# Optimization experiments

Measured on AMD Instinct MI355X. Metric: run time of the kernel, lower is better.

Reference implementation:

```python
import jax, jax.numpy as jnp
import numpy as np

HEADS = 4
DIM_HEAD = 128


def setup_inputs() -> dict:
    key = jax.random.key(0)
    k1, k2, k3, k4, k5 = jax.random.split(key, 5)
    dim = 256
    f, h, w = 8, 14, 14
    inner = HEADS * DIM_HEAD
    scale = DIM_HEAD ** -0.5
    fmap = jax.random.normal(k1, (8, dim, f, h, w), dtype=jnp.float32)
    # Conv3d 1x1x1, no bias -> plain channel matmul weight [3*inner, dim]
    W_qkv = jax.random.normal(k2, (3 * inner, dim), dtype=jnp.float32) * (dim ** -0.5)
    pos_f = jax.random.normal(k3, (f, DIM_HEAD), dtype=jnp.float32) * scale
    pos_h = jax.random.normal(k4, (h, DIM_HEAD), dtype=jnp.float32) * scale
    pos_w = jax.random.normal(k5, (w, DIM_HEAD), dtype=jnp.float32) * scale
    return {"fmap": fmap, "W_qkv": W_qkv, "pos_f": pos_f, "pos_h": pos_h, "pos_w": pos_w}


def reference(fmap, W_qkv, pos_f, pos_h, pos_w):
    b, c, f, h, w = fmap.shape
    n = f * h * w
    scale = DIM_HEAD ** -0.5
    # 1x1x1 Conv3d == channel matmul
    qkv = jnp.einsum('bcfhw,oc->bofhw', fmap, W_qkv)  # [b, 3*inner, f, h, w]
    q, k, v = jnp.split(qkv, 3, axis=1)
    # 'b (h d) x y z -> b h (x y z) d'
    def to_heads(t):
        return t.reshape(b, HEADS, DIM_HEAD, n).transpose(0, 1, 3, 2)
    q, k, v = to_heads(q), to_heads(k), to_heads(v)
    q = q * scale
    # additive absolute positional embedding [n, d]
    emb = (pos_f[:, None, None, :] + pos_h[None, :, None, :] + pos_w[None, None, :, :]).reshape(n, DIM_HEAD)
    sim = jnp.einsum('bhid,bhjd->bhij', q, k) + jnp.einsum('bhid,jd->bhij', q, emb)
    attn = jax.nn.softmax(sim, axis=-1)
    out = jnp.einsum('bhij,bhjd->bhid', attn, v)  # [b, heads, n, d]
    # 'b h (x y z) d -> b (h d) x y z'
    out = out.transpose(0, 1, 3, 2).reshape(b, HEADS * DIM_HEAD, f, h, w)
    return out
```

## Files before the change

kernel.cpp:

```cpp
#include <hip/hip_runtime.h>
#include <hip/hip_bf16.h>
#include <cstdint>

#define NPOS 1568
#define NQPAD 1664
#define NKVT 25
#define DHEAD 128
#define DIM 256
#define NHEADS 4
#define SCALE_Q (0.08838834764831845f * 1.4426950408889634f)

typedef __bf16 bf16x8 __attribute__((ext_vector_type(8)));
typedef float f32x4 __attribute__((ext_vector_type(4)));
typedef float f32x16 __attribute__((ext_vector_type(16)));
typedef unsigned short u16;
typedef u16 u16x8 __attribute__((ext_vector_type(8)));

__device__ __forceinline__ u16 f2bf(float x) {
  union { float f; unsigned int u; } v; v.f = x;
  return (u16)((v.u + 0x7FFFu + ((v.u >> 16) & 1u)) >> 16);
}

__device__ __forceinline__ unsigned cvtpk(float a, float b) {
  unsigned r;
  asm("v_cvt_pk_bf16_f32 %0, %1, %2" : "=v"(r) : "v"(a), "v"(b));
  return r;
}

__device__ __forceinline__ void gload_lds16(const void* g, void* s) {
  __builtin_amdgcn_global_load_lds(
      (const __attribute__((address_space(1))) unsigned*)g,
      (__attribute__((address_space(3))) unsigned*)s, 16, 0, 0);
}

__device__ __forceinline__ f32x16 zero16() {
  f32x16 v;
#pragma unroll
  for (int i = 0; i < 16; ++i) v[i] = 0.f;
  return v;
}

__global__ __launch_bounds__(256) void emb_kernel(
    const float* __restrict__ pf, const float* __restrict__ ph,
    const float* __restrict__ pw, float* __restrict__ emb) {
  int idx = blockIdx.x * 256 + threadIdx.x;
  int pos = idx >> 7, d = idx & 127;
  int jf = pos / 196; int r = pos - jf * 196; int jh = r / 14; int jw = r - jh * 14;
  emb[idx] = pf[jf * 128 + d] + ph[jh * 128 + d] + pw[jw * 128 + d];
}

__device__ __forceinline__ bf16x8 lds_frag64(const u16* base, int row, int ks, int l15, int g) {
  int r = row + l15;
  int off = r * 128 + ((ks * 64 + g * 16) ^ ((r & 7) << 4));
  return *(const bf16x8*)((const char*)base + off);
}

union PSMem {
  struct { u16 wt[64 * 64]; u16 xt[64 * 64]; } s;
  float o_lds[64 * 68];
};

__global__ __launch_bounds__(256) void proj_kernel(
    const float* __restrict__ fmap, const float* __restrict__ W,
    const float* __restrict__ emb, u16* __restrict__ qws, char* __restrict__ tiles) {
  __shared__ PSMem sm;
  const int tid = threadIdx.x;
  const int lane = tid & 63, w = tid >> 6, l15 = lane & 15, g = lane >> 4;
  const int pos0 = blockIdx.x * 64, o0 = blockIdx.y * 64, b = blockIdx.z;

  f32x4 acc[4];
#pragma unroll
  for (int t = 0; t < 4; ++t) acc[t] = (f32x4){0.f, 0.f, 0.f, 0.f};

  for (int c0 = 0; c0 < DIM; c0 += 64) {
    {
      int r = tid >> 2, c16 = (tid & 3) * 16;
      const float* src = W + (o0 + r) * DIM + c0 + c16;
      float4 f0 = *(const float4*)(src + 0);
      float4 f1 = *(const float4*)(src + 4);
      float4 f2 = *(const float4*)(src + 8);
      float4 f3 = *(const float4*)(src + 12);
      u16x8 a, bvv;
      a[0]=f2bf(f0.x); a[1]=f2bf(f0.y); a[2]=f2bf(f0.z); a[3]=f2bf(f0.w);
      a[4]=f2bf(f1.x); a[5]=f2bf(f1.y); a[6]=f2bf(f1.z); a[7]=f2bf(f1.w);
      bvv[0]=f2bf(f2.x); bvv[1]=f2bf(f2.y); bvv[2]=f2bf(f2.z); bvv[3]=f2bf(f2.w);
      bvv[4]=f2bf(f3.x); bvv[5]=f2bf(f3.y); bvv[6]=f2bf(f3.z); bvv[7]=f2bf(f3.w);
      int byte0 = r * 128 + ((c16 * 2) ^ ((r & 7) << 4));
      int byte1 = r * 128 + ((c16 * 2 + 16) ^ ((r & 7) << 4));
      *(u16x8*)((char*)sm.s.wt + byte0) = a;
      *(u16x8*)((char*)sm.s.wt + byte1) = bvv;
    }
#pragma unroll
    for (int it = 0; it < 2; ++it) {
      int cl = (tid >> 3) + it * 32;
      int p8 = (tid & 7) * 8;
      int gp = pos0 + p8;
      if (gp > NPOS - 8) gp = NPOS - 8;
      const float* src = fmap + ((size_t)(b * DIM + c0 + cl)) * NPOS + gp;
      float4 f0 = *(const float4*)(src + 0);
      float4 f1 = *(const float4*)(src + 4);
      float vals[8] = {f0.x, f0.y, f0.z, f0.w, f1.x, f1.y, f1.z, f1.w};
#pragma unroll
      for (int i = 0; i < 8; ++i) {
        int pl = p8 + i;
        int byte = pl * 128 + ((cl * 2) ^ ((pl & 7) << 4));
        *(u16*)((char*)sm.s.xt + byte) = f2bf(vals[i]);
      }
    }
    __syncthreads();
#pragma unroll
    for (int ks = 0; ks < 2; ++ks) {
      bf16x8 aw = lds_frag64(sm.s.wt, w * 16, ks, l15, g);
#pragma unroll
      for (int t = 0; t < 4; ++t) {
        bf16x8 bx = lds_frag64(sm.s.xt, t * 16, ks, l15, g);
        acc[t] = __builtin_amdgcn_mfma_f32_16x16x32_bf16(aw, bx, acc[t], 0, 0, 0);
      }
    }
    __syncthreads();
  }

  const int sec = o0 >> 9;
  const int head = (o0 >> 7) & 3;
  const int dbase = o0 & 127;
  const int bh = b * NHEADS + head;

  if (sec < 2) {
#pragma unroll
    for (int t = 0; t < 4; ++t)
#pragma unroll
      for (int r = 0; r < 4; ++r)
        sm.o_lds[(t * 16 + l15) * 68 + (w * 16 + 4 * g + r)] = acc[t][r];
  } else {
#pragma unroll
    for (int t = 0; t < 4; ++t)
#pragma unroll
      for (int r = 0; r < 4; ++r)
        sm.o_lds[(w * 16 + 4 * g + r) * 68 + (t * 16 + l15)] = acc[t][r];
  }
  __syncthreads();

  if (sec == 0) {
#pragma unroll
    for (int it = 0; it < 2; ++it) {
      int cid = tid + it * 256;
      int p = cid >> 3, c8 = (cid & 7) * 8;
      int gpos = pos0 + p;
      u16x8 o;
      if (gpos < NPOS) {
#pragma unroll
        for (int i = 0; i < 8; ++i) o[i] = f2bf(sm.o_lds[p * 68 + c8 + i] * SCALE_Q);
      } else {
#pragma unroll
        for (int i = 0; i < 8; ++i) o[i] = 0;
      }
      *(u16x8*)(qws + ((size_t)bh * NQPAD + gpos) * DHEAD + dbase + c8) = o;
    }
  } else if (sec == 1) {
    if (pos0 < NKVT * 64) {
#pragma unroll
      for (int it = 0; it < 2; ++it) {
        int cid = tid + it * 256;
        int p = cid >> 3, c8 = (cid & 7) * 8;
        int gpos = pos0 + p;
        u16x8 o;
        if (gpos < NPOS) {
          const float* eb = emb + (size_t)gpos * DHEAD + dbase + c8;
#pragma unroll
          for (int i = 0; i < 8; ++i) o[i] = f2bf(sm.o_lds[p * 68 + c8 + i] + eb[i]);
        } else {
#pragma unroll
          for (int i = 0; i < 8; ++i) o[i] = 0;
        }
        int jt = gpos >> 6, jl = gpos & 63;
        char* dst = tiles + ((size_t)(bh * NKVT + jt)) * 32768 + jl * 256 +
                    (((dbase + c8) * 2) ^ ((jl & 7) << 4));
        *(u16x8*)dst = o;
      }
    }
  } else {
    if (pos0 < NKVT * 64) {
      int jt = pos0 >> 6;
#pragma unroll
      for (int it = 0; it < 2; ++it) {
        int cid = tid + it * 256;
        int r = cid >> 3, p8 = (cid & 7) * 8;
        int d = dbase + r;
        u16x8 o;
        if (pos0 + p8 < NPOS) {
#pragma unroll
          for (int i = 0; i < 8; ++i) o[i] = f2bf(sm.o_lds[r * 68 + p8 + i]);
        } else {
#pragma unroll
          for (int i = 0; i < 8; ++i) o[i] = 0;
        }
        char* dst = tiles + ((size_t)(bh * NKVT + jt)) * 32768 + 16384 + d * 128 +
                    ((p8 * 2) ^ ((d & 7) << 4));
        *(u16x8*)dst = o;
      }
    }
  }
}

__global__ __launch_bounds__(256) void attn_kernel(
    const u16* __restrict__ qws, const char* __restrict__ tiles,
    float* __restrict__ out) {
  __shared__ char smem[65536];
  const int tid = threadIdx.x;
  const int lane = tid & 63, w = tid >> 6;
  const int l31 = lane & 31, hi = lane >> 5;
  const int bh = blockIdx.y, b = bh >> 2, h = bh & 3;
  const int q0 = blockIdx.x * 128;
  const int rho = (l31 & 0x13) | ((l31 & 4) << 1) | ((l31 & 8) >> 1);

  bf16x8 qf[8];
  {
    const u16* qp = qws + ((size_t)bh * NQPAD + q0 + w * 32 + l31) * DHEAD + 8 * hi;
#pragma unroll
    for (int kk = 0; kk < 8; ++kk) qf[kk] = *(const bf16x8*)(qp + kk * 16);
  }

  f32x16 oacc[4];
#pragma unroll
  for (int dt = 0; dt < 4; ++dt) oacc[dt] = zero16();
  float m = -1e30f, l = 0.f;

  const size_t tbase = (size_t)bh * NKVT * 32768;

  {
    const char* src = tiles + tbase + w * 8192 + lane * 16;
    char* dst = smem + w * 8192;
#pragma unroll
    for (int i = 0; i < 8; ++i) gload_lds16(src + i * 1024, dst + i * 1024);
  }
  __syncthreads();

  int cur = 0;
  for (int jt = 0; jt < NKVT; ++jt) {
    if (jt + 1 < NKVT) {
      const char* src = tiles + tbase + (size_t)(jt + 1) * 32768 + w * 8192 + lane * 16;
      char* dst = smem + (cur ^ 1) * 32768 + w * 8192;
#pragma unroll
      for (int i = 0; i < 8; ++i) gload_lds16(src + i * 1024, dst + i * 1024);
    }
    const char* kt = smem + cur * 32768;
    const char* vt = kt + 16384;
    const bool full = (jt < NKVT - 1);

    f32x16 sc0 = zero16(), sc1 = zero16();
    {
      int row = rho, swz = (row & 7) << 4;
#pragma unroll
      for (int kk = 0; kk < 8; ++kk) {
        bf16x8 ka = *(const bf16x8*)(kt + row * 256 + ((kk * 32 + 16 * hi) ^ swz));
        sc0 = __builtin_amdgcn_mfma_f32_32x32x16_bf16(ka, qf[kk], sc0, 0, 0, 0);
      }
    }
    if (full) {
      int row = 32 + rho, swz = (row & 7) << 4;
#pragma unroll
      for (int kk = 0; kk < 8; ++kk) {
        bf16x8 ka = *(const bf16x8*)(kt + row * 256 + ((kk * 32 + 16 * hi) ^ swz));
        sc1 = __builtin_amdgcn_mfma_f32_32x32x16_bf16(ka, qf[kk], sc1, 0, 0, 0);
      }
    }

    float pm = -1e30f;
#pragma unroll
    for (int i = 0; i < 16; ++i) pm = fmaxf(pm, sc0[i]);
    if (full) {
#pragma unroll
      for (int i = 0; i < 16; ++i) pm = fmaxf(pm, sc1[i]);
    }
    pm = fmaxf(pm, __shfl_xor(pm, 32));
    if (!__all(pm <= m + 8.f)) {
      float mn = fmaxf(m, pm);
      float al = exp2f(m - mn);
      m = mn;
      l *= al;
#pragma unroll
      for (int dt = 0; dt < 4; ++dt)
#pragma unroll
        for (int i = 0; i < 16; ++i) oacc[dt][i] *= al;
    }
    float lac = 0.f;
#pragma unroll
    for (int i = 0; i < 16; ++i) { sc0[i] = exp2f(sc0[i] - m); lac += sc0[i]; }
    if (full) {
#pragma unroll
      for (int i = 0; i < 16; ++i) { sc1[i] = exp2f(sc1[i] - m); lac += sc1[i]; }
    }
    l += lac;

    {
      union { unsigned u[4]; bf16x8 v; } pb0, pb1;
      pb0.u[0] = cvtpk(sc0[0], sc0[1]);  pb0.u[1] = cvtpk(sc0[2], sc0[3]);
      pb0.u[2] = cvtpk(sc0[4], sc0[5]);  pb0.u[3] = cvtpk(sc0[6], sc0[7]);
      pb1.u[0] = cvtpk(sc0[8], sc0[9]);  pb1.u[1] = cvtpk(sc0[10], sc0[11]);
      pb1.u[2] = cvtpk(sc0[12], sc0[13]); pb1.u[3] = cvtpk(sc0[14], sc0[15]);
#pragma unroll
      for (int dt = 0; dt < 4; ++dt) {
        int row = dt * 32 + l31, swz = (row & 7) << 4;
        bf16x8 va0 = *(const bf16x8*)(vt + row * 128 + ((16 * hi) ^ swz));
        oacc[dt] = __builtin_amdgcn_mfma_f32_32x32x16_bf16(va0, pb0.v, oacc[dt], 0, 0, 0);
        bf16x8 va1 = *(const bf16x8*)(vt + row * 128 + ((32 + 16 * hi) ^ swz));
        oacc[dt] = __builtin_amdgcn_mfma_f32_32x32x16_bf16(va1, pb1.v, oacc[dt], 0, 0, 0);
      }
    }
    if (full) {
      union { unsigned u[4]; bf16x8 v; } pb0, pb1;
      pb0.u[0] = cvtpk(sc1[0], sc1[1]);  pb0.u[1] = cvtpk(sc1[2], sc1[3]);
      pb0.u[2] = cvtpk(sc1[4], sc1[5]);  pb0.u[3] = cvtpk(sc1[6], sc1[7]);
      pb1.u[0] = cvtpk(sc1[8], sc1[9]);  pb1.u[1] = cvtpk(sc1[10], sc1[11]);
      pb1.u[2] = cvtpk(sc1[12], sc1[13]); pb1.u[3] = cvtpk(sc1[14], sc1[15]);
#pragma unroll
      for (int dt = 0; dt < 4; ++dt) {
        int row = dt * 32 + l31, swz = (row & 7) << 4;
        bf16x8 va0 = *(const bf16x8*)(vt + row * 128 + ((64 + 16 * hi) ^ swz));
        oacc[dt] = __builtin_amdgcn_mfma_f32_32x32x16_bf16(va0, pb0.v, oacc[dt], 0, 0, 0);
        bf16x8 va1 = *(const bf16x8*)(vt + row * 128 + ((96 + 16 * hi) ^ swz));
        oacc[dt] = __builtin_amdgcn_mfma_f32_32x32x16_bf16(va1, pb1.v, oacc[dt], 0, 0, 0);
      }
    }
    __syncthreads();
    cur ^= 1;
  }

  float lt = l + __shfl_xor(l, 32);
  float linv = 1.f / lt;
  const int q = q0 + w * 32 + l31;
  if (q < NPOS) {
    float* ob = out + (size_t)(b * 512 + h * 128) * NPOS + q;
#pragma unroll
    for (int dt = 0; dt < 4; ++dt)
#pragma unroll
      for (int r = 0; r < 16; ++r) {
        int d = dt * 32 + (r & 3) + 8 * (r >> 2) + 4 * hi;
        ob[(size_t)d * NPOS] = oacc[dt][r] * linv;
      }
  }
}

extern "C" void kernel_launch(void* const* d_in, const int* in_sizes, int n_in,
                              void* d_out, int out_size, void* d_ws, size_t ws_size,
                              hipStream_t stream) {
  const float* fmap = (const float*)d_in[0];
  const float* W    = (const float*)d_in[1];
  const float* pf   = (const float*)d_in[2];
  const float* ph   = (const float*)d_in[3];
  const float* pw   = (const float*)d_in[4];
  float* out = (float*)d_out;

  char* ws = (char*)d_ws;
  const size_t QSZ = (size_t)32 * NQPAD * DHEAD * 2;
  const size_t TSZ = (size_t)32 * NKVT * 32768;
  u16* qws = (u16*)ws;
  char* tiles = ws + QSZ;
  float* emb = (float*)(ws + QSZ + TSZ);

  emb_kernel<<<dim3(784), dim3(256), 0, stream>>>(pf, ph, pw, emb);
  proj_kernel<<<dim3(26, 24, 8), dim3(256), 0, stream>>>(fmap, W, emb, qws, tiles);
  attn_kernel<<<dim3(13, 32), dim3(256), 0, stream>>>(qws, tiles, out);
}
```

Baseline: 137.1 us.

## Pre-convert operands, enlarge projection tiles, split attention KV across warp groups

Adds kernels that convert W to bf16 and transpose fmap into a position-major bf16 layout, staged in the output buffer as scratch. The projection GEMM becomes a 128x128 tile per block that loads MFMA fragments straight from global memory, with no LDS staging or per-chunk barriers. The attention kernel moves to 512 threads, and two warp groups each take half of every KV tile; their softmax states and accumulators are merged through LDS at the end. Block indices are also remapped for batch interleaving. This targets conversion overhead and raises parallelism in attention, at the cost of extra launches, a final merge step, and reliance on output-buffer scratch being overwritten in time.

```diff
diff --git a/kernel.cpp b/kernel.cpp
--- a/kernel.cpp
+++ b/kernel.cpp
@@ -7,7 +7,6 @@
 #define NKVT 25
 #define DHEAD 128
 #define DIM 256
-#define NHEADS 4
 #define SCALE_Q (0.08838834764831845f * 1.4426950408889634f)
 
 typedef __bf16 bf16x8 __attribute__((ext_vector_type(8)));
@@ -15,11 +14,6 @@
 typedef float f32x16 __attribute__((ext_vector_type(16)));
 typedef unsigned short u16;
 typedef u16 u16x8 __attribute__((ext_vector_type(8)));
-
-__device__ __forceinline__ u16 f2bf(float x) {
-  union { float f; unsigned int u; } v; v.f = x;
-  return (u16)((v.u + 0x7FFFu + ((v.u >> 16) & 1u)) >> 16);
-}
 
 __device__ __forceinline__ unsigned cvtpk(float a, float b) {
   unsigned r;
@@ -49,173 +43,200 @@
   emb[idx] = pf[jf * 128 + d] + ph[jh * 128 + d] + pw[jw * 128 + d];
 }
 
-__device__ __forceinline__ bf16x8 lds_frag64(const u16* base, int row, int ks, int l15, int g) {
-  int r = row + l15;
-  int off = r * 128 + ((ks * 64 + g * 16) ^ ((r & 7) << 4));
-  return *(const bf16x8*)((const char*)base + off);
-}
-
-union PSMem {
-  struct { u16 wt[64 * 64]; u16 xt[64 * 64]; } s;
-  float o_lds[64 * 68];
-};
-
-__global__ __launch_bounds__(256) void proj_kernel(
-    const float* __restrict__ fmap, const float* __restrict__ W,
+__global__ __launch_bounds__(256) void wconv_kernel(
+    const float* __restrict__ W, u16* __restrict__ Wbf) {
+  int i8 = (blockIdx.x * 256 + threadIdx.x) * 8;
+  float4 f0 = *(const float4*)(W + i8);
+  float4 f1 = *(const float4*)(W + i8 + 4);
+  union { unsigned u[4]; u16x8 v; } o;
+  o.u[0] = cvtpk(f0.x, f0.y); o.u[1] = cvtpk(f0.z, f0.w);
+  o.u[2] = cvtpk(f1.x, f1.y); o.u[3] = cvtpk(f1.z, f1.w);
+  *(u16x8*)(Wbf + i8) = o.v;
+}
+
+__global__ __launch_bounds__(256) void ftrans_kernel(
+    const float* __restrict__ fmap, u16* __restrict__ fmapT) {
+  __shared__ float t[64][68];
+  const int tid = threadIdx.x;
+  const int pos0 = blockIdx.x * 64, c0 = blockIdx.y * 64, b = blockIdx.z;
+  const int cl = tid >> 3, p8 = (tid & 7) * 8;
+  const bool pv = (pos0 + p8) < NPOS;
+#pragma unroll
+  for (int half = 0; half < 2; ++half) {
+    int c = cl + half * 32;
+    float4 f0 = {0.f, 0.f, 0.f, 0.f}, f1 = {0.f, 0.f, 0.f, 0.f};
+    if (pv) {
+      const float* src = fmap + ((size_t)(b * DIM + c0 + c)) * NPOS + pos0 + p8;
+      f0 = *(const float4*)src;
+      f1 = *(const float4*)(src + 4);
+    }
+    *(float4*)&t[c][p8] = f0;
+    *(float4*)&t[c][p8 + 4] = f1;
+  }
+  __syncthreads();
+  const int pl = tid >> 2, c16 = (tid & 3) * 16;
+  const int gpos = pos0 + pl;
+  union { unsigned u[8]; } o;
+  if (gpos < NPOS) {
+#pragma unroll
+    for (int i = 0; i < 8; ++i) o.u[i] = cvtpk(t[c16 + 2 * i][pl], t[c16 + 2 * i + 1][pl]);
+  } else {
+#pragma unroll
+    for (int i = 0; i < 8; ++i) o.u[i] = 0;
+  }
+  u16* dst = fmapT + ((size_t)b * NQPAD + gpos) * DIM + c0 + c16;
+  *(uint4*)(dst) = *(uint4*)&o.u[0];
+  *(uint4*)(dst + 8) = *(uint4*)&o.u[4];
+}
+
+__global__ __launch_bounds__(256, 4) void proj_kernel(
+    const u16* __restrict__ Wbf, const u16* __restrict__ fmapT,
     const float* __restrict__ emb, u16* __restrict__ qws, char* __restrict__ tiles) {
-  __shared__ PSMem sm;
+  __shared__ float ot[64][132];
   const int tid = threadIdx.x;
-  const int lane = tid & 63, w = tid >> 6, l15 = lane & 15, g = lane >> 4;
-  const int pos0 = blockIdx.x * 64, o0 = blockIdx.y * 64, b = blockIdx.z;
-
-  f32x4 acc[4];
-#pragma unroll
-  for (int t = 0; t < 4; ++t) acc[t] = (f32x4){0.f, 0.f, 0.f, 0.f};
-
-  for (int c0 = 0; c0 < DIM; c0 += 64) {
-    {
-      int r = tid >> 2, c16 = (tid & 3) * 16;
-      const float* src = W + (o0 + r) * DIM + c0 + c16;
-      float4 f0 = *(const float4*)(src + 0);
-      float4 f1 = *(const float4*)(src + 4);
-      float4 f2 = *(const float4*)(src + 8);
-      float4 f3 = *(const float4*)(src + 12);
-      u16x8 a, bvv;
-      a[0]=f2bf(f0.x); a[1]=f2bf(f0.y); a[2]=f2bf(f0.z); a[3]=f2bf(f0.w);
-      a[4]=f2bf(f1.x); a[5]=f2bf(f1.y); a[6]=f2bf(f1.z); a[7]=f2bf(f1.w);
-      bvv[0]=f2bf(f2.x); bvv[1]=f2bf(f2.y); bvv[2]=f2bf(f2.z); bvv[3]=f2bf(f2.w);
-      bvv[4]=f2bf(f3.x); bvv[5]=f2bf(f3.y); bvv[6]=f2bf(f3.z); bvv[7]=f2bf(f3.w);
-      int byte0 = r * 128 + ((c16 * 2) ^ ((r & 7) << 4));
-      int byte1 = r * 128 + ((c16 * 2 + 16) ^ ((r & 7) << 4));
-      *(u16x8*)((char*)sm.s.wt + byte0) = a;
-      *(u16x8*)((char*)sm.s.wt + byte1) = bvv;
-    }
-#pragma unroll
-    for (int it = 0; it < 2; ++it) {
-      int cl = (tid >> 3) + it * 32;
-      int p8 = (tid & 7) * 8;
-      int gp = pos0 + p8;
-      if (gp > NPOS - 8) gp = NPOS - 8;
-      const float* src = fmap + ((size_t)(b * DIM + c0 + cl)) * NPOS + gp;
-      float4 f0 = *(const float4*)(src + 0);
-      float4 f1 = *(const float4*)(src + 4);
-      float vals[8] = {f0.x, f0.y, f0.z, f0.w, f1.x, f1.y, f1.z, f1.w};
-#pragma unroll
-      for (int i = 0; i < 8; ++i) {
-        int pl = p8 + i;
-        int byte = pl * 128 + ((cl * 2) ^ ((pl & 7) << 4));
-        *(u16*)((char*)sm.s.xt + byte) = f2bf(vals[i]);
-      }
-    }
-    __syncthreads();
-#pragma unroll
-    for (int ks = 0; ks < 2; ++ks) {
-      bf16x8 aw = lds_frag64(sm.s.wt, w * 16, ks, l15, g);
-#pragma unroll
-      for (int t = 0; t < 4; ++t) {
-        bf16x8 bx = lds_frag64(sm.s.xt, t * 16, ks, l15, g);
-        acc[t] = __builtin_amdgcn_mfma_f32_16x16x32_bf16(aw, bx, acc[t], 0, 0, 0);
-      }
-    }
-    __syncthreads();
-  }
-
-  const int sec = o0 >> 9;
-  const int head = (o0 >> 7) & 3;
-  const int dbase = o0 & 127;
-  const int bh = b * NHEADS + head;
+  const int lane = tid & 63, w = tid >> 6;
+  const int l15 = lane & 15, g = lane >> 4;
+  const int wid = blockIdx.x;
+  const int b = wid & 7;
+  const int gq = wid >> 3;
+  const int o0 = (gq / 13) * 128;
+  const int pos0 = (gq % 13) * 128;
+  const int wo = (w & 1) * 64, wp = (w >> 1) * 64;
+
+  f32x4 acc[4][4];
+#pragma unroll
+  for (int i = 0; i < 4; ++i)
+#pragma unroll
+    for (int j = 0; j < 4; ++j) acc[i][j] = (f32x4){0.f, 0.f, 0.f, 0.f};
+
+  const u16* Ab = Wbf + (size_t)(o0 + wo + l15) * DIM + g * 8;
+  const u16* Bb = fmapT + ((size_t)b * NQPAD + pos0 + wp + l15) * DIM + g * 8;
+#pragma unroll 2
+  for (int c0 = 0; c0 < DIM; c0 += 32) {
+    bf16x8 a[4], bb[4];
+#pragma unroll
+    for (int t = 0; t < 4; ++t) a[t] = *(const bf16x8*)(Ab + (size_t)t * 16 * DIM + c0);
+#pragma unroll
+    for (int t = 0; t < 4; ++t) bb[t] = *(const bf16x8*)(Bb + (size_t)t * 16 * DIM + c0);
+#pragma unroll
+    for (int i = 0; i < 4; ++i)
+#pragma unroll
+      for (int j = 0; j < 4; ++j)
+        acc[i][j] = __builtin_amdgcn_mfma_f32_16x16x32_bf16(a[i], bb[j], acc[i][j], 0, 0, 0);
+  }
+
+  const int sec = o0 >> 9, head = (o0 >> 7) & 3, bh = b * 4 + head;
 
   if (sec < 2) {
 #pragma unroll
-    for (int t = 0; t < 4; ++t)
-#pragma unroll
-      for (int r = 0; r < 4; ++r)
-        sm.o_lds[(t * 16 + l15) * 68 + (w * 16 + 4 * g + r)] = acc[t][r];
+    for (int ph = 0; ph < 2; ++ph) {
+      __syncthreads();
+      if (wp == ph * 64) {
+#pragma unroll
+        for (int i = 0; i < 4; ++i)
+#pragma unroll
+          for (int j = 0; j < 4; ++j)
+#pragma unroll
+            for (int r = 0; r < 4; ++r)
+              ot[j * 16 + l15][wo + i * 16 + 4 * g + r] = acc[i][j][r];
+      }
+      __syncthreads();
+      const int pl = tid >> 2, c32 = (tid & 3) * 32;
+      const int gpos = pos0 + ph * 64 + pl;
+      float v[32];
+#pragma unroll
+      for (int i = 0; i < 32; ++i) v[i] = ot[pl][c32 + i];
+      if (sec == 0) {
+#pragma unroll
+        for (int q = 0; q < 4; ++q) {
+          union { unsigned u[4]; u16x8 h; } o8;
+#pragma unroll
+          for (int i = 0; i < 4; ++i)
+            o8.u[i] = cvtpk(v[q * 8 + 2 * i] * SCALE_Q, v[q * 8 + 2 * i + 1] * SCALE_Q);
+          *(u16x8*)(qws + ((size_t)bh * NQPAD + gpos) * DHEAD + c32 + q * 8) = o8.h;
+        }
+      } else {
+        if (gpos < NKVT * 64) {
+          if (gpos < NPOS) {
+            const float* eb = emb + (size_t)gpos * DHEAD + c32;
+#pragma unroll
+            for (int i = 0; i < 8; ++i) {
+              float4 e = *(const float4*)(eb + i * 4);
+              v[i * 4 + 0] += e.x; v[i * 4 + 1] += e.y;
+              v[i * 4 + 2] += e.z; v[i * 4 + 3] += e.w;
+            }
+          }
+          const int jt = gpos >> 6, jl = gpos & 63;
+          char* base = tiles + ((size_t)(bh * NKVT + jt)) * 32768 + jl * 256;
+          const int swz = (jl & 7) << 4;
+#pragma unroll
+          for (int q = 0; q < 4; ++q) {
+            union { unsigned u[4]; u16x8 h; } o8;
+#pragma unroll
+            for (int i = 0; i < 4; ++i)
+              o8.u[i] = cvtpk(v[q * 8 + 2 * i], v[q * 8 + 2 * i + 1]);
+            *(u16x8*)(base + (((c32 + q * 8) * 2) ^ swz)) = o8.h;
+          }
+        }
+      }
+    }
   } else {
 #pragma unroll
-    for (int t = 0; t < 4; ++t)
-#pragma unroll
-      for (int r = 0; r < 4; ++r)
-        sm.o_lds[(w * 16 + 4 * g + r) * 68 + (t * 16 + l15)] = acc[t][r];
-  }
-  __syncthreads();
-
-  if (sec == 0) {
-#pragma unroll
-    for (int it = 0; it < 2; ++it) {
-      int cid = tid + it * 256;
-      int p = cid >> 3, c8 = (cid & 7) * 8;
-      int gpos = pos0 + p;
-      u16x8 o;
-      if (gpos < NPOS) {
-#pragma unroll
-        for (int i = 0; i < 8; ++i) o[i] = f2bf(sm.o_lds[p * 68 + c8 + i] * SCALE_Q);
-      } else {
-#pragma unroll
-        for (int i = 0; i < 8; ++i) o[i] = 0;
-      }
-      *(u16x8*)(qws + ((size_t)bh * NQPAD + gpos) * DHEAD + dbase + c8) = o;
-    }
-  } else if (sec == 1) {
-    if (pos0 < NKVT * 64) {
-#pragma unroll
-      for (int it = 0; it < 2; ++it) {
-        int cid = tid + it * 256;
-        int p = cid >> 3, c8 = (cid & 7) * 8;
-        int gpos = pos0 + p;
-        u16x8 o;
-        if (gpos < NPOS) {
-          const float* eb = emb + (size_t)gpos * DHEAD + dbase + c8;
-#pragma unroll
-          for (int i = 0; i < 8; ++i) o[i] = f2bf(sm.o_lds[p * 68 + c8 + i] + eb[i]);
-        } else {
-#pragma unroll
-          for (int i = 0; i < 8; ++i) o[i] = 0;
-        }
-        int jt = gpos >> 6, jl = gpos & 63;
-        char* dst = tiles + ((size_t)(bh * NKVT + jt)) * 32768 + jl * 256 +
-                    (((dbase + c8) * 2) ^ ((jl & 7) << 4));
-        *(u16x8*)dst = o;
-      }
-    }
-  } else {
-    if (pos0 < NKVT * 64) {
-      int jt = pos0 >> 6;
-#pragma unroll
-      for (int it = 0; it < 2; ++it) {
-        int cid = tid + it * 256;
-        int r = cid >> 3, p8 = (cid & 7) * 8;
-        int d = dbase + r;
-        u16x8 o;
-        if (pos0 + p8 < NPOS) {
-#pragma unroll
-          for (int i = 0; i < 8; ++i) o[i] = f2bf(sm.o_lds[r * 68 + p8 + i]);
-        } else {
-#pragma unroll
-          for (int i = 0; i < 8; ++i) o[i] = 0;
-        }
-        char* dst = tiles + ((size_t)(bh * NKVT + jt)) * 32768 + 16384 + d * 128 +
-                    ((p8 * 2) ^ ((d & 7) << 4));
-        *(u16x8*)dst = o;
-      }
-    }
-  }
-}
-
-__global__ __launch_bounds__(256) void attn_kernel(
+    for (int ch = 0; ch < 2; ++ch) {
+      __syncthreads();
+      if (wo == ch * 64) {
+#pragma unroll
+        for (int i = 0; i < 4; ++i)
+#pragma unroll
+          for (int j = 0; j < 4; ++j)
+#pragma unroll
+            for (int r = 0; r < 4; ++r)
+              ot[i * 16 + 4 * g + r][wp + j * 16 + l15] = acc[i][j][r];
+      }
+      __syncthreads();
+      const int dl = tid >> 2, p32 = (tid & 3) * 32;
+      const int d = ch * 64 + dl;
+      const int gp = pos0 + p32;
+      float v[32];
+#pragma unroll
+      for (int i = 0; i < 32; ++i) v[i] = ot[dl][p32 + i];
+      if (gp < NKVT * 64) {
+        const int jt = gp >> 6, jl0 = gp & 63;
+        char* base = tiles + ((size_t)(bh * NKVT + jt)) * 32768 + 16384 + d * 128;
+        const int swz = (d & 7) << 4;
+#pragma unroll
+        for (int q = 0; q < 4; ++q) {
+          union { unsigned u[4]; u16x8 h; } o8;
+#pragma unroll
+          for (int i = 0; i < 4; ++i)
+            o8.u[i] = cvtpk(v[q * 8 + 2 * i], v[q * 8 + 2 * i + 1]);
+          *(u16x8*)(base + (((jl0 + q * 8) * 2) ^ swz)) = o8.h;
+        }
+      }
+    }
+  }
+}
+
+__global__ __launch_bounds__(512, 4) void attn_kernel(
     const u16* __restrict__ qws, const char* __restrict__ tiles,
     float* __restrict__ out) {
   __shared__ char smem[65536];
   const int tid = threadIdx.x;
   const int lane = tid & 63, w = tid >> 6;
+  const int qw = w & 3, grp = w >> 2;
   const int l31 = lane & 31, hi = lane >> 5;
-  const int bh = blockIdx.y, b = bh >> 2, h = bh & 3;
-  const int q0 = blockIdx.x * 128;
+  const int wid = blockIdx.x;
+  const int bh = (wid & 7) * 4 + (wid >> 3) / 13;
+  const int bx = (wid >> 3) % 13;
+  const int b = bh >> 2, h = bh & 3;
+  const int q0 = bx * 128;
   const int rho = (l31 & 0x13) | ((l31 & 4) << 1) | ((l31 & 8) >> 1);
+  const int krow = grp * 32 + rho;
+  const int jb = grp * 64;
 
   bf16x8 qf[8];
   {
-    const u16* qp = qws + ((size_t)bh * NQPAD + q0 + w * 32 + l31) * DHEAD + 8 * hi;
+    const u16* qp = qws + ((size_t)bh * NQPAD + q0 + qw * 32 + l31) * DHEAD + 8 * hi;
 #pragma unroll
     for (int kk = 0; kk < 8; ++kk) qf[kk] = *(const bf16x8*)(qp + kk * 16);
   }
@@ -228,97 +249,64 @@
   const size_t tbase = (size_t)bh * NKVT * 32768;
 
   {
-    const char* src = tiles + tbase + w * 8192 + lane * 16;
-    char* dst = smem + w * 8192;
-#pragma unroll
-    for (int i = 0; i < 8; ++i) gload_lds16(src + i * 1024, dst + i * 1024);
+    const char* src = tiles + tbase + w * 4096 + lane * 16;
+    char* dst = smem + w * 4096;
+#pragma unroll
+    for (int i = 0; i < 4; ++i) gload_lds16(src + i * 1024, dst + i * 1024);
   }
   __syncthreads();
 
   int cur = 0;
   for (int jt = 0; jt < NKVT; ++jt) {
     if (jt + 1 < NKVT) {
-      const char* src = tiles + tbase + (size_t)(jt + 1) * 32768 + w * 8192 + lane * 16;
-      char* dst = smem + (cur ^ 1) * 32768 + w * 8192;
-#pragma unroll
-      for (int i = 0; i < 8; ++i) gload_lds16(src + i * 1024, dst + i * 1024);
+      const char* src = tiles + tbase + (size_t)(jt + 1) * 32768 + w * 4096 + lane * 16;
+      char* dst = smem + (cur ^ 1) * 32768 + w * 4096;
+#pragma unroll
+      for (int i = 0; i < 4; ++i) gload_lds16(src + i * 1024, dst + i * 1024);
     }
     const char* kt = smem + cur * 32768;
     const char* vt = kt + 16384;
-    const bool full = (jt < NKVT - 1);
-
-    f32x16 sc0 = zero16(), sc1 = zero16();
-    {
-      int row = rho, swz = (row & 7) << 4;
-#pragma unroll
-      for (int kk = 0; kk < 8; ++kk) {
-        bf16x8 ka = *(const bf16x8*)(kt + row * 256 + ((kk * 32 + 16 * hi) ^ swz));
-        sc0 = __builtin_amdgcn_mfma_f32_32x32x16_bf16(ka, qf[kk], sc0, 0, 0, 0);
-      }
-    }
-    if (full) {
-      int row = 32 + rho, swz = (row & 7) << 4;
-#pragma unroll
-      for (int kk = 0; kk < 8; ++kk) {
-        bf16x8 ka = *(const bf16x8*)(kt + row * 256 + ((kk * 32 + 16 * hi) ^ swz));
-        sc1 = __builtin_amdgcn_mfma_f32_32x32x16_bf16(ka, qf[kk], sc1, 0, 0, 0);
-      }
-    }
-
-    float pm = -1e30f;
-#pragma unroll
-    for (int i = 0; i < 16; ++i) pm = fmaxf(pm, sc0[i]);
-    if (full) {
-#pragma unroll
-      for (int i = 0; i < 16; ++i) pm = fmaxf(pm, sc1[i]);
-    }
-    pm = fmaxf(pm, __shfl_xor(pm, 32));
-    if (!__all(pm <= m + 8.f)) {
-      float mn = fmaxf(m, pm);
-      float al = exp2f(m - mn);
-      m = mn;
-      l *= al;
-#pragma unroll
-      for (int dt = 0; dt < 4; ++dt)
-#pragma unroll
-        for (int i = 0; i < 16; ++i) oacc[dt][i] *= al;
-    }
-    float lac = 0.f;
-#pragma unroll
-    for (int i = 0; i < 16; ++i) { sc0[i] = exp2f(sc0[i] - m); lac += sc0[i]; }
-    if (full) {
-#pragma unroll
-      for (int i = 0; i < 16; ++i) { sc1[i] = exp2f(sc1[i] - m); lac += sc1[i]; }
-    }
-    l += lac;
-
-    {
+
+    if (grp == 0 || jt < NKVT - 1) {
+      f32x16 sc = zero16();
+      {
+        const int swz = (krow & 7) << 4;
+#pragma unroll
+        for (int kk = 0; kk < 8; ++kk) {
+          bf16x8 ka = *(const bf16x8*)(kt + krow * 256 + ((kk * 32 + 16 * hi) ^ swz));
+          sc = __builtin_amdgcn_mfma_f32_32x32x16_bf16(ka, qf[kk], sc, 0, 0, 0);
+        }
+      }
+      float pm = -1e30f;
+#pragma unroll
+      for (int i = 0; i < 16; ++i) pm = fmaxf(pm, sc[i]);
+      pm = fmaxf(pm, __shfl_xor(pm, 32));
+      if (!__all(pm <= m + 8.f)) {
+        float mn = fmaxf(m, pm);
+        float al = exp2f(m - mn);
+        m = mn;
+        l *= al;
+#pragma unroll
+        for (int dt = 0; dt < 4; ++dt)
+#pragma unroll
+          for (int i = 0; i < 16; ++i) oacc[dt][i] *= al;
+      }
+      float lac = 0.f;
+#pragma unroll
+      for (int i = 0; i < 16; ++i) { sc[i] = exp2f(sc[i] - m); lac += sc[i]; }
+      l += lac;
+
       union { unsigned u[4]; bf16x8 v; } pb0, pb1;
-      pb0.u[0] = cvtpk(sc0[0], sc0[1]);  pb0.u[1] = cvtpk(sc0[2], sc0[3]);
-      pb0.u[2] = cvtpk(sc0[4], sc0[5]);  pb0.u[3] = cvtpk(sc0[6], sc0[7]);
-      pb1.u[0] = cvtpk(sc0[8], sc0[9]);  pb1.u[1] = cvtpk(sc0[10], sc0[11]);
-      pb1.u[2] = cvtpk(sc0[12], sc0[13]); pb1.u[3] = cvtpk(sc0[14], sc0[15]);
+      pb0.u[0] = cvtpk(sc[0], sc[1]);   pb0.u[1] = cvtpk(sc[2], sc[3]);
+      pb0.u[2] = cvtpk(sc[4], sc[5]);   pb0.u[3] = cvtpk(sc[6], sc[7]);
+      pb1.u[0] = cvtpk(sc[8], sc[9]);   pb1.u[1] = cvtpk(sc[10], sc[11]);
+      pb1.u[2] = cvtpk(sc[12], sc[13]); pb1.u[3] = cvtpk(sc[14], sc[15]);
 #pragma unroll
       for (int dt = 0; dt < 4; ++dt) {
-        int row = dt * 32 + l31, swz = (row & 7) << 4;
-        bf16x8 va0 = *(const bf16x8*)(vt + row * 128 + ((16 * hi) ^ swz));
+        const int row = dt * 32 + l31, swz = (row & 7) << 4;
+        bf16x8 va0 = *(const bf16x8*)(vt + row * 128 + ((jb + 16 * hi) ^ swz));
         oacc[dt] = __builtin_amdgcn_mfma_f32_32x32x16_bf16(va0, pb0.v, oacc[dt], 0, 0, 0);
-        bf16x8 va1 = *(const bf16x8*)(vt + row * 128 + ((32 + 16 * hi) ^ swz));
-        oacc[dt] = __builtin_amdgcn_mfma_f32_32x32x16_bf16(va1, pb1.v, oacc[dt], 0, 0, 0);
-      }
-    }
-    if (full) {
-      union { unsigned u[4]; bf16x8 v; } pb0, pb1;
-      pb0.u[0] = cvtpk(sc1[0], sc1[1]);  pb0.u[1] = cvtpk(sc1[2], sc1[3]);
-      pb0.u[2] = cvtpk(sc1[4], sc1[5]);  pb0.u[3] = cvtpk(sc1[6], sc1[7]);
-      pb1.u[0] = cvtpk(sc1[8], sc1[9]);  pb1.u[1] = cvtpk(sc1[10], sc1[11]);
-      pb1.u[2] = cvtpk(sc1[12], sc1[13]); pb1.u[3] = cvtpk(sc1[14], sc1[15]);
-#pragma unroll
-      for (int dt = 0; dt < 4; ++dt) {
-        int row = dt * 32 + l31, swz = (row & 7) << 4;
-        bf16x8 va0 = *(const bf16x8*)(vt + row * 128 + ((64 + 16 * hi) ^ swz));
-        oacc[dt] = __builtin_amdgcn_mfma_f32_32x32x16_bf16(va0, pb0.v, oacc[dt], 0, 0, 0);
-        bf16x8 va1 = *(const bf16x8*)(vt + row * 128 + ((96 + 16 * hi) ^ swz));
+        bf16x8 va1 = *(const bf16x8*)(vt + row * 128 + ((jb + 32 + 16 * hi) ^ swz));
         oacc[dt] = __builtin_amdgcn_mfma_f32_32x32x16_bf16(va1, pb1.v, oacc[dt], 0, 0, 0);
       }
     }
@@ -327,17 +315,48 @@
   }
 
   float lt = l + __shfl_xor(l, 32);
-  float linv = 1.f / lt;
-  const int q = q0 + w * 32 + l31;
-  if (q < NPOS) {
-    float* ob = out + (size_t)(b * 512 + h * 128) * NPOS + q;
-#pragma unroll
-    for (int dt = 0; dt < 4; ++dt)
-#pragma unroll
-      for (int r = 0; r < 16; ++r) {
-        int d = dt * 32 + (r & 3) + 8 * (r >> 2) + 4 * hi;
-        ob[(size_t)d * NPOS] = oacc[dt][r] * linv;
-      }
+  float* ml = (float*)smem;
+  float* cx = (float*)(smem + 4096);
+  if (grp == 1) {
+    ml[(qw * 64 + lane) * 2 + 0] = m;
+    ml[(qw * 64 + lane) * 2 + 1] = lt;
+  }
+  __syncthreads();
+  float fA = 0.f, fB = 0.f;
+  if (grp == 0) {
+    float mB = ml[(qw * 64 + lane) * 2 + 0];
+    float lB = ml[(qw * 64 + lane) * 2 + 1];
+    float ms = fmaxf(m, mB);
+    float aA = exp2f(m - ms), aB = exp2f(mB - ms);
+    float inv = 1.f / (lt * aA + lB * aB);
+    fA = aA * inv; fB = aB * inv;
+  }
+  const int q = q0 + qw * 32 + l31;
+  float* ob = out + (size_t)(b * 512 + h * 128) * NPOS + q;
+#pragma unroll
+  for (int ch = 0; ch < 2; ++ch) {
+    __syncthreads();
+    if (grp == 1) {
+#pragma unroll
+      for (int k = 0; k < 2; ++k)
+#pragma unroll
+        for (int i = 0; i < 16; ++i)
+          cx[(k * 16 + i) * 256 + qw * 64 + lane] = oacc[ch * 2 + k][i];
+    }
+    __syncthreads();
+    if (grp == 0 && q < NPOS) {
+#pragma unroll
+      for (int k = 0; k < 2; ++k) {
+        const int dt = ch * 2 + k;
+#pragma unroll
+        for (int r = 0; r < 16; ++r) {
+          float vB = cx[(k * 16 + r) * 256 + qw * 64 + lane];
+          float vo = oacc[dt][r] * fA + vB * fB;
+          int d = dt * 32 + (r & 3) + 8 * (r >> 2) + 4 * hi;
+          ob[(size_t)d * NPOS] = vo;
+        }
+      }
+    }
   }
 }
 
@@ -353,12 +372,19 @@
 
   char* ws = (char*)d_ws;
   const size_t QSZ = (size_t)32 * NQPAD * DHEAD * 2;
-  const size_t TSZ = (size_t)32 * NKVT * 32768;
-  u16* qws = (u16*)ws;
+  u16* qws    = (u16*)ws;
   char* tiles = ws + QSZ;
-  float* emb = (float*)(ws + QSZ + TSZ);
+
+  char* oscr = (char*)d_out;
+  const size_t FSZ = (size_t)8 * NQPAD * DIM * 2;
+  const size_t WSZ = (size_t)1536 * DIM * 2;
+  u16* fmapT = (u16*)oscr;
+  u16* Wbf   = (u16*)(oscr + FSZ);
+  float* emb = (float*)(oscr + FSZ + WSZ);
 
   emb_kernel<<<dim3(784), dim3(256), 0, stream>>>(pf, ph, pw, emb);
-  proj_kernel<<<dim3(26, 24, 8), dim3(256), 0, stream>>>(fmap, W, emb, qws, tiles);
-  attn_kernel<<<dim3(13, 32), dim3(256), 0, stream>>>(qws, tiles, out);
-}
+  wconv_kernel<<<dim3(192), dim3(256), 0, stream>>>(W, Wbf);
+  ftrans_kernel<<<dim3(26, 4, 8), dim3(256), 0, stream>>>(fmap, fmapT);
+  proj_kernel<<<dim3(1248), dim3(256), 0, stream>>>(Wbf, fmapT, emb, qws, tiles);
+  attn_kernel<<<dim3(416), dim3(512), 0, stream>>>(qws, tiles, out);
+}
```

New measurement: 152.5 us. 11.2% more time.
